# Performance work log

Hardware: AMD Instinct MI355X
Metric: run time of the kernel (lower is better)

Reference implementation:

```python
import jax, jax.numpy as jnp
import numpy as np

EPS = 1e-7  # SimplifiedLayerNorm eps


def setup_inputs() -> dict:
    key = jax.random.key(0)
    k1, k2 = jax.random.split(key)
    x = jax.random.normal(k1, (8, 2048, 64), dtype=jnp.float32)   # [B, T, d]
    W = jax.random.normal(k2, (2048, 8), dtype=jnp.float32)       # [T, H] per-distance, per-head Toeplitz weights
    return {"x": x, "W": W}


def _l2norm(v):
    return v / (jnp.linalg.norm(v, axis=-1, keepdims=True) + EPS)


def reference(x, W):
    B, T, d = x.shape
    H = W.shape[1]
    # pad one zero token: [B, T+1, d]
    xp = jnp.concatenate([x, jnp.zeros((B, 1, d), x.dtype)], axis=1)
    idx = jnp.arange(T + 1)
    dist = idx[:, None] - idx[None, :]                 # [T+1, T+1], row - col
    # Toeplitz logits: W[dist, h] for 0 <= dist < T; the single dist==T entry
    # (bottom-left corner) is left at its initial 0.0; dist < 0 is causally masked.
    Wd = W[jnp.clip(dist, 0, T - 1)]                   # [T+1, T+1, H]
    dist3 = dist[..., None]
    logits = jnp.where(dist3 < 0, -jnp.inf,
                       jnp.where(dist3 >= T, jnp.zeros((), x.dtype), Wd))
    probs = jax.nn.softmax(logits, axis=1)             # softmax over columns (dim=-1 of W_h)
    v = jnp.einsum('tsh,bsd->hbtd', probs, xp)         # [H, B, T+1, d]
    v = _l2norm(v)
    V = jnp.concatenate([v, xp[None]], axis=0)         # [H+1, B, T+1, d]
    V = _l2norm(V)
    return V
```

## Files before the change

### kernel.cpp

```cpp
#include <hip/hip_runtime.h>

#define EPS 1e-7f
#define T_DIM 2048
#define TP1   2049
#define H_DIM 8
#define B_DIM 8
#define D_DIM 64
#define SP    2080
#define NFRAG 134
#define FB_OFF 32

typedef short v8s __attribute__((ext_vector_type(8)));
typedef float v4f __attribute__((ext_vector_type(4)));

static __device__ __forceinline__ unsigned short f2bf(float f) {
  union { float f; unsigned u; } v; v.f = f;
  unsigned r = v.u + 0x7fffu + ((v.u >> 16) & 1u);
  return (unsigned short)(r >> 16);
}

__global__ __launch_bounds__(64) void build_fragA(const float* __restrict__ W,
                                                  unsigned short* __restrict__ fragA) {
  const int blk = blockIdx.x;
  const int h = blk / NFRAG, fb = blk - h * NFRAG;
  const int b0 = fb * 16 - FB_OFF;
  const int lane = threadIdx.x;
  const int lm = lane & 15, quad = lane >> 4;
  v8s frag;
  #pragma unroll
  for (int j = 0; j < 8; ++j) {
    int d = b0 + lm - 8 * quad - j;
    float v = 0.0f;
    if (d >= 0 && d < T_DIM) v = __expf(W[d * H_DIM + h]);
    else if (d == T_DIM) v = 1.0f;
    frag[j] = (short)f2bf(v);
  }
  *(v8s*)(fragA + ((size_t)(blk * 64 + lane)) * 8) = frag;
}

__global__ __launch_bounds__(256) void transpose_x(const float* __restrict__ x,
                                                   unsigned short* __restrict__ xT) {
  int b = blockIdx.x / 33, st = blockIdx.x % 33;
  int tid = threadIdx.x;
  if (st == 32) {
    #pragma unroll
    for (int i = 0; i < 8; ++i) {
      int idx = tid * 8 + i;
      int dd = idx >> 5, sl = idx & 31;
      xT[((size_t)b * D_DIM + dd) * SP + T_DIM + sl] = 0;
    }
    return;
  }
  __shared__ float tile[64][65];
  int s0 = st * 64;
  int c = tid & 63, r4 = tid >> 6;
  #pragma unroll
  for (int i = 0; i < 16; ++i) {
    int sl = r4 * 16 + i;
    tile[sl][c] = x[((size_t)b * T_DIM + (s0 + sl)) * D_DIM + c];
  }
  __syncthreads();
  #pragma unroll
  for (int i = 0; i < 16; ++i) {
    int dd = r4 * 16 + i;
    xT[((size_t)b * D_DIM + dd) * SP + s0 + c] = f2bf(tile[c][dd]);
  }
}

__global__ __launch_bounds__(64) void toeplitz_mm(const unsigned short* __restrict__ fragA,
                                                  const unsigned short* __restrict__ xT,
                                                  float* __restrict__ out) {
  const int lane = threadIdx.x;
  const int lm   = lane & 15;
  const int quad = lane >> 4;

  const int bi  = blockIdx.x;
  const int tt  = 32 - (bi >> 6);
  const int rem = bi & 63;
  const int h = rem >> 3, b = rem & 7;
  const int t0 = tt * 64;

  const unsigned short* fA = fragA + ((size_t)h * NFRAG * 64 + lane) * 8;
  const unsigned short* xb = xT + (size_t)b * D_DIM * SP;

  v4f acc[4][4] = {};

  const int s_end = min(t0 + 32, T_DIM);

  auto loadA = [&](int mt, int s0) -> v8s {
    int fb = (t0 + 16 * mt - s0 + FB_OFF) >> 4;
    return *(const v8s*)(fA + (size_t)fb * 64 * 8);
  };
  auto loadB = [&](int nt, int s0) -> v8s {
    const unsigned short* p = xb + (size_t)(16 * nt + lm) * SP + s0 + 8 * quad;
    return *(const v8s*)p;
  };

  v8s fa[4], fbr[4];
  #pragma unroll
  for (int mt = 0; mt < 4; ++mt) fa[mt] = loadA(mt, 0);
  #pragma unroll
  for (int nt = 0; nt < 4; ++nt) fbr[nt] = loadB(nt, 0);

  for (int s0 = 0;; s0 += 32) {
    const bool more = s0 < s_end;
    v8s na0, na1, nb[4];
    if (more) {
      #pragma unroll
      for (int nt = 0; nt < 4; ++nt) nb[nt] = loadB(nt, s0 + 32);
      na0 = loadA(0, s0 + 32);
      na1 = loadA(1, s0 + 32);
    }
    #pragma unroll
    for (int mt = 0; mt < 4; ++mt)
      #pragma unroll
      for (int nt = 0; nt < 4; ++nt)
        acc[mt][nt] = __builtin_amdgcn_mfma_f32_16x16x32_bf16(fa[mt], fbr[nt], acc[mt][nt], 0, 0, 0);
    if (!more) break;
    fa[3] = fa[1]; fa[2] = fa[0]; fa[1] = na1; fa[0] = na0;
    #pragma unroll
    for (int nt = 0; nt < 4; ++nt) fbr[nt] = nb[nt];
  }

  #pragma unroll
  for (int mt = 0; mt < 4; ++mt) {
    #pragma unroll
    for (int r = 0; r < 4; ++r) {
      float ss = 0.0f;
      #pragma unroll
      for (int nt = 0; nt < 4; ++nt) { float a = acc[mt][nt][r]; ss += a * a; }
      ss += __shfl_xor(ss, 1);
      ss += __shfl_xor(ss, 2);
      ss += __shfl_xor(ss, 4);
      ss += __shfl_xor(ss, 8);
      int t = t0 + 16 * mt + 4 * quad + r;
      if (t <= T_DIM) {
        float n1 = sqrtf(ss);
        float u  = n1 / (n1 + EPS);
        float inv = 1.0f / ((n1 + EPS) * (u + EPS));
        float* op = out + (((size_t)(h * B_DIM + b) * TP1 + t) << 6) + lm;
        #pragma unroll
        for (int nt = 0; nt < 4; ++nt) op[16 * nt] = acc[mt][nt][r] * inv;
      }
    }
  }
}

__global__ __launch_bounds__(256) void xhat_out(const float* __restrict__ x,
                                               float* __restrict__ out) {
  int row = blockIdx.x * 4 + (threadIdx.x >> 6);
  if (row >= B_DIM * TP1) return;
  int b = row / TP1, t = row - b * TP1;
  int dd = threadIdx.x & 63;
  float v = (t < T_DIM) ? x[((size_t)b * T_DIM + t) * D_DIM + dd] : 0.0f;
  float ss = v * v;
  ss += __shfl_xor(ss, 1);
  ss += __shfl_xor(ss, 2);
  ss += __shfl_xor(ss, 4);
  ss += __shfl_xor(ss, 8);
  ss += __shfl_xor(ss, 16);
  ss += __shfl_xor(ss, 32);
  float inv = 1.0f / (sqrtf(ss) + EPS);
  out[(((size_t)(H_DIM * B_DIM + b) * TP1 + t) << 6) + dd] = v * inv;
}

extern "C" void kernel_launch(void* const* d_in, const int* in_sizes, int n_in,
                              void* d_out, int out_size, void* d_ws, size_t ws_size,
                              hipStream_t stream) {
  const float* x = (const float*)d_in[0];
  const float* W = (const float*)d_in[1];
  float* out = (float*)d_out;

  unsigned short* xT    = (unsigned short*)d_ws;
  unsigned short* fragA = (unsigned short*)((char*)d_ws + 2131968);

  hipLaunchKernelGGL(build_fragA, dim3(H_DIM * NFRAG), dim3(64), 0, stream, W, fragA);
  hipLaunchKernelGGL(transpose_x, dim3(B_DIM * 33), dim3(256), 0, stream, x, xT);
  hipLaunchKernelGGL(toeplitz_mm, dim3(64 * 33), dim3(64), 0, stream, fragA, xT, out);
  hipLaunchKernelGGL(xhat_out, dim3((B_DIM * TP1 + 3) / 4), dim3(256), 0, stream, x, out);
}
```

Baseline: 126.2 us.

## Split Toeplitz K-loop across four waves and merge prep kernels into one launch

```diff
diff --git a/kernel.cpp b/kernel.cpp
--- a/kernel.cpp
+++ b/kernel.cpp
@@ -5,10 +5,10 @@
 #define TP1   2049
 #define H_DIM 8
 #define B_DIM 8
-#define D_DIM 64
 #define SP    2080
 #define NFRAG 134
 #define FB_OFF 32
+#define RSTRIDE 66
 
 typedef short v8s __attribute__((ext_vector_type(8)));
 typedef float v4f __attribute__((ext_vector_type(4)));
@@ -19,58 +19,87 @@
   return (unsigned short)(r >> 16);
 }
 
-__global__ __launch_bounds__(64) void build_fragA(const float* __restrict__ W,
-                                                  unsigned short* __restrict__ fragA) {
-  const int blk = blockIdx.x;
-  const int h = blk / NFRAG, fb = blk - h * NFRAG;
-  const int b0 = fb * 16 - FB_OFF;
-  const int lane = threadIdx.x;
-  const int lm = lane & 15, quad = lane >> 4;
-  v8s frag;
-  #pragma unroll
-  for (int j = 0; j < 8; ++j) {
-    int d = b0 + lm - 8 * quad - j;
-    float v = 0.0f;
-    if (d >= 0 && d < T_DIM) v = __expf(W[d * H_DIM + h]);
-    else if (d == T_DIM) v = 1.0f;
-    frag[j] = (short)f2bf(v);
-  }
-  *(v8s*)(fragA + ((size_t)(blk * 64 + lane)) * 8) = frag;
-}
-
-__global__ __launch_bounds__(256) void transpose_x(const float* __restrict__ x,
-                                                   unsigned short* __restrict__ xT) {
-  int b = blockIdx.x / 33, st = blockIdx.x % 33;
-  int tid = threadIdx.x;
-  if (st == 32) {
-    #pragma unroll
-    for (int i = 0; i < 8; ++i) {
-      int idx = tid * 8 + i;
-      int dd = idx >> 5, sl = idx & 31;
-      xT[((size_t)b * D_DIM + dd) * SP + T_DIM + sl] = 0;
-    }
+#define J1_BLOCKS 268
+#define J2_BLOCKS 264
+#define J3_BLOCKS 4098
+
+__global__ __launch_bounds__(256) void prep(const float* __restrict__ x,
+                                            const float* __restrict__ W,
+                                            unsigned short* __restrict__ fragA,
+                                            unsigned short* __restrict__ xT,
+                                            float* __restrict__ out) {
+  __shared__ float tile[64][65];
+  int bid = blockIdx.x;
+  if (bid < J1_BLOCKS) {
+    int tid = bid * 256 + threadIdx.x;
+    int blk = tid >> 6, lane = tid & 63;
+    int h = blk / NFRAG, fb = blk - h * NFRAG;
+    int b0 = fb * 16 - FB_OFF;
+    int lm = lane & 15, quad = lane >> 4;
+    v8s frag;
+    #pragma unroll
+    for (int j = 0; j < 8; ++j) {
+      int d = b0 + lm - 8 * quad - j;
+      float v = 0.0f;
+      if (d >= 0 && d < T_DIM) v = __expf(W[d * H_DIM + h]);
+      else if (d == T_DIM) v = 1.0f;
+      frag[j] = (short)f2bf(v);
+    }
+    *(v8s*)(fragA + (size_t)tid * 8) = frag;
     return;
   }
-  __shared__ float tile[64][65];
-  int s0 = st * 64;
-  int c = tid & 63, r4 = tid >> 6;
-  #pragma unroll
-  for (int i = 0; i < 16; ++i) {
-    int sl = r4 * 16 + i;
-    tile[sl][c] = x[((size_t)b * T_DIM + (s0 + sl)) * D_DIM + c];
-  }
-  __syncthreads();
-  #pragma unroll
-  for (int i = 0; i < 16; ++i) {
-    int dd = r4 * 16 + i;
-    xT[((size_t)b * D_DIM + dd) * SP + s0 + c] = f2bf(tile[c][dd]);
-  }
-}
-
-__global__ __launch_bounds__(64) void toeplitz_mm(const unsigned short* __restrict__ fragA,
-                                                  const unsigned short* __restrict__ xT,
-                                                  float* __restrict__ out) {
-  const int lane = threadIdx.x;
+  bid -= J1_BLOCKS;
+  if (bid < J2_BLOCKS) {
+    int b = bid / 33, st = bid % 33;
+    int tid = threadIdx.x;
+    if (st == 32) {
+      #pragma unroll
+      for (int i = 0; i < 8; ++i) {
+        int idx = tid * 8 + i;
+        int dd = idx >> 5, sl = idx & 31;
+        xT[((size_t)b * 64 + dd) * SP + T_DIM + sl] = 0;
+      }
+      return;
+    }
+    int s0 = st * 64;
+    int c = tid & 63, r4 = tid >> 6;
+    #pragma unroll
+    for (int i = 0; i < 16; ++i) {
+      int sl = r4 * 16 + i;
+      tile[sl][c] = x[((size_t)b * T_DIM + (s0 + sl)) * 64 + c];
+    }
+    __syncthreads();
+    #pragma unroll
+    for (int i = 0; i < 16; ++i) {
+      int dd = r4 * 16 + i;
+      xT[((size_t)b * 64 + dd) * SP + s0 + c] = f2bf(tile[c][dd]);
+    }
+    return;
+  }
+  bid -= J2_BLOCKS;
+  {
+    int row = bid * 4 + (threadIdx.x >> 6);
+    if (row >= B_DIM * TP1) return;
+    int b = row / TP1, t = row - b * TP1;
+    int dd = threadIdx.x & 63;
+    float v = (t < T_DIM) ? x[((size_t)b * T_DIM + t) * 64 + dd] : 0.0f;
+    float ss = v * v;
+    ss += __shfl_xor(ss, 1);  ss += __shfl_xor(ss, 2);
+    ss += __shfl_xor(ss, 4);  ss += __shfl_xor(ss, 8);
+    ss += __shfl_xor(ss, 16); ss += __shfl_xor(ss, 32);
+    float inv = 1.0f / (sqrtf(ss) + EPS);
+    out[(((size_t)(H_DIM * B_DIM + b) * TP1 + t) << 6) + dd] = v * inv;
+  }
+}
+
+__global__ __launch_bounds__(256) void toeplitz_mm(const unsigned short* __restrict__ fragA,
+                                                   const unsigned short* __restrict__ xT,
+                                                   float* __restrict__ out) {
+  __shared__ float bufA[64 * RSTRIDE];
+  __shared__ float bufB[64 * RSTRIDE];
+
+  const int lane = threadIdx.x & 63;
+  const int w    = threadIdx.x >> 6;
   const int lm   = lane & 15;
   const int quad = lane >> 4;
 
@@ -81,46 +110,76 @@
   const int t0 = tt * 64;
 
   const unsigned short* fA = fragA + ((size_t)h * NFRAG * 64 + lane) * 8;
-  const unsigned short* xb = xT + (size_t)b * D_DIM * SP;
+  const unsigned short* xb = xT + ((size_t)b * 64 + lm) * SP + 8 * quad;
+
+  const int s_end = min(t0 + 32, T_DIM);
 
   v4f acc[4][4] = {};
 
-  const int s_end = min(t0 + 32, T_DIM);
-
-  auto loadA = [&](int mt, int s0) -> v8s {
-    int fb = (t0 + 16 * mt - s0 + FB_OFF) >> 4;
-    return *(const v8s*)(fA + (size_t)fb * 64 * 8);
-  };
-  auto loadB = [&](int nt, int s0) -> v8s {
-    const unsigned short* p = xb + (size_t)(16 * nt + lm) * SP + s0 + 8 * quad;
-    return *(const v8s*)p;
-  };
-
-  v8s fa[4], fbr[4];
-  #pragma unroll
-  for (int mt = 0; mt < 4; ++mt) fa[mt] = loadA(mt, 0);
-  #pragma unroll
-  for (int nt = 0; nt < 4; ++nt) fbr[nt] = loadB(nt, 0);
-
-  for (int s0 = 0;; s0 += 32) {
-    const bool more = s0 < s_end;
-    v8s na0, na1, nb[4];
-    if (more) {
-      #pragma unroll
-      for (int nt = 0; nt < 4; ++nt) nb[nt] = loadB(nt, s0 + 32);
-      na0 = loadA(0, s0 + 32);
-      na1 = loadA(1, s0 + 32);
-    }
-    #pragma unroll
-    for (int mt = 0; mt < 4; ++mt)
-      #pragma unroll
-      for (int nt = 0; nt < 4; ++nt)
-        acc[mt][nt] = __builtin_amdgcn_mfma_f32_16x16x32_bf16(fa[mt], fbr[nt], acc[mt][nt], 0, 0, 0);
-    if (!more) break;
-    fa[3] = fa[1]; fa[2] = fa[0]; fa[1] = na1; fa[0] = na0;
-    #pragma unroll
-    for (int nt = 0; nt < 4; ++nt) fbr[nt] = nb[nt];
-  }
+  v8s a0[4], a1[4], b0[4], b1[4];
+
+#define LOAD_A(dst, s0v) do {                                        \
+    const v8s* _p = (const v8s*)(fA + (size_t)(((t0 - (s0v) + FB_OFF) >> 4)) * 512); \
+    dst[0] = _p[0]; dst[1] = _p[64]; dst[2] = _p[128]; dst[3] = _p[192]; } while (0)
+#define LOAD_B(dst, s0v) do {                                        \
+    const unsigned short* _p = xb + (s0v);                           \
+    dst[0] = *(const v8s*)(_p);                                      \
+    dst[1] = *(const v8s*)(_p + 16 * SP);                            \
+    dst[2] = *(const v8s*)(_p + 32 * SP);                            \
+    dst[3] = *(const v8s*)(_p + 48 * SP); } while (0)
+#define DO_MFMA(fa, fb) do {                                         \
+    _Pragma("unroll")                                                \
+    for (int mt = 0; mt < 4; ++mt)                                   \
+      _Pragma("unroll")                                              \
+      for (int nt = 0; nt < 4; ++nt)                                 \
+        acc[mt][nt] = __builtin_amdgcn_mfma_f32_16x16x32_bf16(fa[mt], fb[nt], acc[mt][nt], 0, 0, 0); } while (0)
+
+  int s0 = 32 * w;
+  if (s0 <= s_end) {
+    LOAD_A(a0, s0); LOAD_B(b0, s0);
+    for (;;) {
+      bool more = (s0 + 128 <= s_end);
+      if (more) { LOAD_A(a1, s0 + 128); LOAD_B(b1, s0 + 128); }
+      DO_MFMA(a0, b0);
+      if (!more) break;
+      s0 += 128;
+      bool more2 = (s0 + 128 <= s_end);
+      if (more2) { LOAD_A(a0, s0 + 128); LOAD_B(b0, s0 + 128); }
+      DO_MFMA(a1, b1);
+      if (!more2) break;
+      s0 += 128;
+    }
+  }
+
+#define ST_ACC(buf) do {                                             \
+    _Pragma("unroll")                                                \
+    for (int mt = 0; mt < 4; ++mt)                                   \
+      _Pragma("unroll")                                              \
+      for (int r = 0; r < 4; ++r) {                                  \
+        int row = 16 * mt + 4 * quad + r;                            \
+        _Pragma("unroll")                                            \
+        for (int nt = 0; nt < 4; ++nt)                               \
+          buf[row * RSTRIDE + 16 * nt + lm] = acc[mt][nt][r]; } } while (0)
+#define ADD_ACC(buf) do {                                            \
+    _Pragma("unroll")                                                \
+    for (int mt = 0; mt < 4; ++mt)                                   \
+      _Pragma("unroll")                                              \
+      for (int r = 0; r < 4; ++r) {                                  \
+        int row = 16 * mt + 4 * quad + r;                            \
+        _Pragma("unroll")                                            \
+        for (int nt = 0; nt < 4; ++nt)                               \
+          acc[mt][nt][r] += buf[row * RSTRIDE + 16 * nt + lm]; } } while (0)
+
+  if (w == 1) ST_ACC(bufA);
+  if (w == 3) ST_ACC(bufB);
+  __syncthreads();
+  if (w == 0) ADD_ACC(bufA);
+  if (w == 2) ADD_ACC(bufB);
+  __syncthreads();
+  if (w == 2) ST_ACC(bufA);
+  __syncthreads();
+  if (w != 0) return;
+  ADD_ACC(bufA);
 
   #pragma unroll
   for (int mt = 0; mt < 4; ++mt) {
@@ -146,24 +205,6 @@
   }
 }
 
-__global__ __launch_bounds__(256) void xhat_out(const float* __restrict__ x,
-                                               float* __restrict__ out) {
-  int row = blockIdx.x * 4 + (threadIdx.x >> 6);
-  if (row >= B_DIM * TP1) return;
-  int b = row / TP1, t = row - b * TP1;
-  int dd = threadIdx.x & 63;
-  float v = (t < T_DIM) ? x[((size_t)b * T_DIM + t) * D_DIM + dd] : 0.0f;
-  float ss = v * v;
-  ss += __shfl_xor(ss, 1);
-  ss += __shfl_xor(ss, 2);
-  ss += __shfl_xor(ss, 4);
-  ss += __shfl_xor(ss, 8);
-  ss += __shfl_xor(ss, 16);
-  ss += __shfl_xor(ss, 32);
-  float inv = 1.0f / (sqrtf(ss) + EPS);
-  out[(((size_t)(H_DIM * B_DIM + b) * TP1 + t) << 6) + dd] = v * inv;
-}
-
 extern "C" void kernel_launch(void* const* d_in, const int* in_sizes, int n_in,
                               void* d_out, int out_size, void* d_ws, size_t ws_size,
                               hipStream_t stream) {
@@ -174,8 +215,7 @@
   unsigned short* xT    = (unsigned short*)d_ws;
   unsigned short* fragA = (unsigned short*)((char*)d_ws + 2131968);
 
-  hipLaunchKernelGGL(build_fragA, dim3(H_DIM * NFRAG), dim3(64), 0, stream, W, fragA);
-  hipLaunchKernelGGL(transpose_x, dim3(B_DIM * 33), dim3(256), 0, stream, x, xT);
-  hipLaunchKernelGGL(toeplitz_mm, dim3(64 * 33), dim3(64), 0, stream, fragA, xT, out);
-  hipLaunchKernelGGL(xhat_out, dim3((B_DIM * TP1 + 3) / 4), dim3(256), 0, stream, x, out);
-}
+  hipLaunchKernelGGL(prep, dim3(J1_BLOCKS + J2_BLOCKS + J3_BLOCKS), dim3(256), 0, stream,
+                     x, W, fragA, xT, out);
+  hipLaunchKernelGGL(toeplitz_mm, dim3(64 * 33), dim3(256), 0, stream, fragA, xT, out);
+}
```

New measurement: 119.0 us. -5.6%, faster.
